# Kernel tuning notes

Measured on AMD Instinct MI355X. Metric: run time of the kernel, lower is better.

The kernel has to match this reference:

```python
import jax, jax.numpy as jnp
import numpy as np

# dims: d=1024 model width, h=16 heads, d_head=64
B, S, D, H = 4, 1024, 1024, 16
RD = float(np.sqrt(D))
VAR_W_INIT = 0.001  # var_init[0]: initial weight-variance value


def setup_inputs() -> dict:
    key = jax.random.key(0)
    ks = jax.random.split(key, 5)
    x = jax.random.normal(ks[0], (B, S, D), jnp.float32)
    # input variance must be non-negative; small positive values
    var_x = jax.random.uniform(ks[1], (B, S, D), jnp.float32) * 0.01
    scale = 1.0 / np.sqrt(D)
    Wq = jax.random.normal(ks[2], (D, D), jnp.float32) * scale
    Wk = jax.random.normal(ks[3], (D, D), jnp.float32) * scale
    Wv = jax.random.normal(ks[4], (D, D), jnp.float32) * scale
    var_Wq = jnp.full((D, D), VAR_W_INIT, jnp.float32)
    var_Wk = jnp.full((D, D), VAR_W_INIT, jnp.float32)
    var_Wv = jnp.full((D, D), VAR_W_INIT, jnp.float32)
    return dict(x=x, var_x=var_x, Wq=Wq, var_Wq=var_Wq, Wk=Wk, var_Wk=var_Wk, Wv=Wv, var_Wv=var_Wv)


def _linear_vmp(x, var_x, W, var_W):
    # mean: x W^T ; variance of product of independent Gaussians:
    # var = var_x (W^2)^T + x^2 var_W^T + var_x var_W^T
    m = x @ W.T
    v = var_x @ (W * W).T + (x * x) @ var_W.T + var_x @ var_W.T
    return m, v


def _quadratic_vmp(m1, v1, m2, v2):
    # matmul of two independent Gaussian tensors (moment propagation)
    m = m1 @ m2
    v = v1 @ v2 + v1 @ (m2 * m2) + (m1 * m1) @ v2
    return m, v


def _softmax_vmp(a, var_a):
    # delta-method through softmax: J_ij = s_i(delta_ij - s_j)
    # var_i = s_i^2 [ (1-2 s_i) var_i + sum_j s_j^2 var_j ]
    s = jax.nn.softmax(a, axis=-1)
    sv = jnp.sum(s * s * var_a, axis=-1, keepdims=True)
    var_s = s * s * ((1.0 - 2.0 * s) * var_a + sv)
    return s, var_s


def _split_heads(t):
    b, s, _ = t.shape
    return t.reshape(b, s, H, D // H).transpose(0, 2, 1, 3)  # [B,H,S,dh]


def reference(x, var_x, Wq, var_Wq, Wk, var_Wk, Wv, var_Wv):
    q, vq = _linear_vmp(x, var_x, Wq, var_Wq)
    k, vk = _linear_vmp(x, var_x, Wk, var_Wk)
    v, vv = _linear_vmp(x, var_x, Wv, var_Wv)
    q, vq, k, vk, v, vv = map(_split_heads, (q, vq, k, vk, v, vv))
    kt = k.transpose(0, 1, 3, 2)
    vkt = vk.transpose(0, 1, 3, 2)
    a, va = _quadratic_vmp(q, vq, kt, vkt)          # [B,H,S,S]
    a, va = a / RD, va / (RD * RD)
    a, va = _softmax_vmp(a, va)                      # masking=False path
    o, vo = _quadratic_vmp(a, va, v, vv)             # [B,H,S,dh]
    o = o.transpose(0, 2, 1, 3).reshape(x.shape)
    vo = vo.transpose(0, 2, 1, 3).reshape(x.shape)
    # residual_vmp, mode='identity': mean add, variances add
    return x + o, var_x + vo
```

## Files before the change

kernel.cpp:

```cpp
#include <hip/hip_runtime.h>
#include <hip/hip_bf16.h>

#define BB 4
#define SS 1024
#define DD 1024
#define HH 16
#define DH 64
#define MM (BB*SS)

typedef __attribute__((ext_vector_type(8))) short bf16x8;
typedef __attribute__((ext_vector_type(8))) unsigned short u16x8;
typedef __attribute__((ext_vector_type(4))) float f32x4;

__device__ __forceinline__ float b2f(unsigned short u) {
    union { unsigned int i; float f; } c; c.i = ((unsigned int)u) << 16; return c.f;
}
__device__ __forceinline__ unsigned short f2b(float f) {
    __hip_bfloat16 h = __float2bfloat16(f);
    return *reinterpret_cast<unsigned short*>(&h);
}
__device__ __forceinline__ unsigned int pack2(float a, float b) {
    unsigned int r;
    asm("v_cvt_pk_bf16_f32 %0, %1, %2" : "=v"(r) : "v"(a), "v"(b));
    return r;
}
__device__ __forceinline__ void gload16(const unsigned short* g, unsigned short* l) {
    __builtin_amdgcn_global_load_lds(
        (const __attribute__((address_space(1))) void*)g,
        (__attribute__((address_space(3))) void*)l,
        16, 0, 0);
}
#define MFMA16(a, b, c) __builtin_amdgcn_mfma_f32_16x16x32_bf16(a, b, c, 0, 0, 0)

__global__ __launch_bounds__(256) void prep_xw_kernel(
    const float* __restrict__ x, const float* __restrict__ vx,
    const float* __restrict__ W0, const float* __restrict__ vW0,
    const float* __restrict__ W1, const float* __restrict__ vW1,
    const float* __restrict__ W2, const float* __restrict__ vW2,
    unsigned short* __restrict__ xb, unsigned short* __restrict__ vxb,
    unsigned short* __restrict__ xsb, unsigned short* __restrict__ wp)
{
    const int gx = blockIdx.x;
    if (gx < 4096) {
        const size_t i = ((size_t)gx * 256 + threadIdx.x) * 4;
        float4 a = *(const float4*)(x + i);
        float4 b = *(const float4*)(vx + i);
        ushort4 oa = { f2b(a.x), f2b(a.y), f2b(a.z), f2b(a.w) };
        ushort4 ob = { f2b(b.x), f2b(b.y), f2b(b.z), f2b(b.w) };
        ushort4 os = { f2b(a.x*a.x), f2b(a.y*a.y), f2b(a.z*a.z), f2b(a.w*a.w) };
        *(ushort4*)(xb  + i) = oa;
        *(ushort4*)(vxb + i) = ob;
        *(ushort4*)(xsb + i) = os;
    } else {
        const int bxx = gx - 4096;
        const int z   = bxx >> 10;
        const int bx  = bxx & 1023;
        const float* W  = (z==0)? W0 : (z==1)? W1 : W2;
        const float* vW = (z==0)? vW0: (z==1)? vW1: vW2;
        const size_t NW = (size_t)DD*DD;
        unsigned short* wb = wp + (size_t)(3*z+0)*NW;
        unsigned short* wc = wp + (size_t)(3*z+1)*NW;
        unsigned short* wv = wp + (size_t)(3*z+2)*NW;
        const size_t i = ((size_t)bx * 256 + threadIdx.x) * 4;
        float4 a = *(const float4*)(W + i);
        float4 b = *(const float4*)(vW + i);
        ushort4 oa = { f2b(a.x), f2b(a.y), f2b(a.z), f2b(a.w) };
        ushort4 oc = { f2b(a.x*a.x + b.x), f2b(a.y*a.y + b.y),
                       f2b(a.z*a.z + b.z), f2b(a.w*a.w + b.w) };
        ushort4 ov = { f2b(b.x), f2b(b.y), f2b(b.z), f2b(b.w) };
        *(ushort4*)(wb + i) = oa;
        *(ushort4*)(wc + i) = oc;
        *(ushort4*)(wv + i) = ov;
    }
}

__global__ __launch_bounds__(256) void gemm_proj_kernel(
    const unsigned short* __restrict__ xb, const unsigned short* __restrict__ vxb,
    const unsigned short* __restrict__ xsb,
    const unsigned short* __restrict__ wp,
    unsigned short* __restrict__ qm, unsigned short* __restrict__ km,
    unsigned short* __restrict__ vm,
    unsigned short* __restrict__ qv, unsigned short* __restrict__ kv,
    unsigned short* __restrict__ vvv)
{
    __shared__ unsigned short sA[2][128*32];
    __shared__ unsigned short sB[2][128*32];

    const int z = blockIdx.z;
    const size_t NW = (size_t)DD*DD;
    const bool isVar = (z >= 3);
    const int p = isVar ? (z - 3) : z;
    const unsigned short* A0 = isVar ? vxb : xb;
    const unsigned short* A1 = isVar ? xsb : xb;
    const unsigned short* B0 = wp + (size_t)(3*p + (isVar ? 1 : 0)) * NW;
    const unsigned short* B1 = isVar ? (wp + (size_t)(3*p + 2) * NW) : B0;
    unsigned short* Out = (z==0)? qm : (z==1)? km : (z==2)? vm
                        : (z==3)? qv : (z==4)? kv : vvv;
    const int NT = isVar ? 64 : 32;

    const int orig = blockIdx.x + (blockIdx.y << 3);
    const int swz  = ((orig & 7) << 5) | (orig >> 3);
    const int bn = swz & 7;
    const int bm = swz >> 3;

    const int tid = threadIdx.x;
    const int w = tid >> 6;
    const int l = tid & 63;
    const int wr = w >> 1, wc = w & 1;

    const int r0 = tid >> 2;
    const int s0 = (((tid & 3) ^ ((r0 >> 1) & 3)) * 8);
    const size_t aoff0 = (size_t)(bm*128 + r0) * DD + s0;
    const size_t boff0 = (size_t)(bn*128 + r0) * DD + s0;
    const int ldsd0 = (w*64) * 8;
    const int ldsd1 = (256 + w*64) * 8;

#define STG(buf, t) do {                                                   \
        const unsigned short* As_ = ((t) < 32) ? A0 : A1;                  \
        const unsigned short* Bs_ = ((t) < 32) ? B0 : B1;                  \
        const int kc_ = ((t) & 31) * 32;                                   \
        gload16(As_ + aoff0 + kc_,                   &sA[buf][ldsd0]);     \
        gload16(As_ + aoff0 + (size_t)64*DD + kc_,   &sA[buf][ldsd1]);     \
        gload16(Bs_ + boff0 + kc_,                   &sB[buf][ldsd0]);     \
        gload16(Bs_ + boff0 + (size_t)64*DD + kc_,   &sB[buf][ldsd1]);     \
    } while (0)

    f32x4 acc[4][4];
    #pragma unroll
    for (int i = 0; i < 4; ++i)
        #pragma unroll
        for (int j = 0; j < 4; ++j)
            acc[i][j] = (f32x4){0.f,0.f,0.f,0.f};

    const int fr = l & 15;
    const int hi = l >> 4;

    STG(0, 0);
    __syncthreads();

    for (int t = 0; t < NT; ++t) {
        const int cb = t & 1;
        if (t + 1 < NT) STG(cb ^ 1, t + 1);

        bf16x8 bfr[4];
        #pragma unroll
        for (int j = 0; j < 4; ++j) {
            const int row = wc*64 + j*16 + fr;
            bfr[j] = *(const bf16x8*)&sB[cb][row*32 + ((hi ^ ((row >> 1) & 3)) * 8)];
        }
        #pragma unroll
        for (int i = 0; i < 4; ++i) {
            const int row = wr*64 + i*16 + fr;
            bf16x8 a0 = *(const bf16x8*)&sA[cb][row*32 + ((hi ^ ((row >> 1) & 3)) * 8)];
            #pragma unroll
            for (int j = 0; j < 4; ++j)
                acc[i][j] = MFMA16(a0, bfr[j], acc[i][j]);
        }
        __syncthreads();
    }
#undef STG

    const int orow = bm*128 + wr*64 + (hi << 2);
    const int ocol = bn*128 + wc*64 + fr;
    #pragma unroll
    for (int i = 0; i < 4; ++i)
        #pragma unroll
        for (int j = 0; j < 4; ++j)
            #pragma unroll
            for (int r = 0; r < 4; ++r)
                Out[(size_t)(orow + i*16 + r) * DD + ocol + j*16] = f2b(acc[i][j][r]);
}

__global__ __launch_bounds__(256) void prep_vtkk_kernel(
    const unsigned short* __restrict__ vm, const unsigned short* __restrict__ vvv,
    const unsigned short* __restrict__ kmp, const unsigned short* __restrict__ kvp,
    unsigned short* __restrict__ vt, unsigned short* __restrict__ wt,
    unsigned short* __restrict__ vvt, unsigned short* __restrict__ kkb)
{
    __shared__ unsigned short tv[64][68];
    __shared__ unsigned short tw[64][68];
    __shared__ unsigned short tvv[64][68];
    const int t = threadIdx.x;
    const int gx = blockIdx.x;

    if (gx >= 1024) {
        const size_t i = ((size_t)(gx - 1024) * 256 + t) * 8;
        u16x8 k8 = *(const u16x8*)(kmp + i);
        u16x8 v8 = *(const u16x8*)(kvp + i);
        u16x8 o8;
        #pragma unroll
        for (int e = 0; e < 8; ++e) {
            float kf = b2f(k8[e]);
            o8[e] = f2b(b2f(v8[e]) + kf*kf);
        }
        *(u16x8*)(kkb + i) = o8;
        return;
    }

    const int jt = gx & 15, h = (gx >> 4) & 15, b = gx >> 8;
    const size_t ibase = (size_t)b*SS*DD + (size_t)h*DH;
    {
        const int j = t & 63, cg = t >> 6;
        const size_t ga = ibase + (size_t)(jt*64 + j)*DD + cg*16;
        #pragma unroll
        for (int hh = 0; hh < 2; ++hh) {
            u16x8 v8  = *(const u16x8*)(vm  + ga + hh*8);
            u16x8 vv8 = *(const u16x8*)(vvv + ga + hh*8);
            u16x8 w8;
            #pragma unroll
            for (int e = 0; e < 8; ++e) {
                float vf = b2f(v8[e]);
                w8[e] = f2b(b2f(vv8[e]) + vf*vf);
            }
            *(u16x8*)&tv[j][cg*16 + hh*8]  = v8;
            *(u16x8*)&tvv[j][cg*16 + hh*8] = vv8;
            *(u16x8*)&tw[j][cg*16 + hh*8]  = w8;
        }
    }
    __syncthreads();
    {
        const int d  = t >> 2;
        const int pc = t & 3;
        const int lc = pc ^ ((d >> 1) & 3);
        #pragma unroll
        for (int st = 0; st < 2; ++st) {
            u16x8 o0, o1, o2;
            #pragma unroll
            for (int e = 0; e < 8; ++e) {
                const int jl = st*32 + (e >> 2)*16 + lc*4 + (e & 3);
                o0[e] = tv[jl][d];
                o1[e] = tw[jl][d];
                o2[e] = tvv[jl][d];
            }
            const size_t ob = (size_t)((b*HH + h)*DH + d)*SS + jt*64 + st*32 + pc*8;
            *(u16x8*)(vt  + ob) = o0;
            *(u16x8*)(wt  + ob) = o1;
            *(u16x8*)(vvt + ob) = o2;
        }
    }
}

union PW { unsigned int u[4]; bf16x8 v; };

__global__ __launch_bounds__(256, 3) void attn_mfma_kernel(
    const unsigned short* __restrict__ kmg, const unsigned short* __restrict__ kvg,
    const unsigned short* __restrict__ kkg,
    const unsigned short* __restrict__ vtg, const unsigned short* __restrict__ wtg,
    const unsigned short* __restrict__ vvtg,
    const unsigned short* __restrict__ qmg, const unsigned short* __restrict__ qvg,
    const float* __restrict__ x, const float* __restrict__ vx,
    float* __restrict__ om, float* __restrict__ ov)
{
    __shared__ unsigned short Ks[2][3][32*64];
    __shared__ unsigned short Vs[2][3][64*32];

    const int tid = threadIdx.x;
    const int w = tid >> 6, l = tid & 63;
    const int lo = l & 15, hi = l >> 4;

    const int fb = blockIdx.x;
    const int g  = ((fb >> 7) << 3) | (fb & 7);
    const int qt = (fb >> 3) & 15;
    const int h  = g & 15;
    const int b  = g >> 4;

    const size_t xbase = (size_t)b*SS*DD + (size_t)h*DH;
    const size_t vbase = (size_t)(b*HH + h)*DH*SS;

    bf16x8 qA[2], vqA[2], qsA[2];
    {
        const int qrow = qt*64 + w*16 + lo;
        #pragma unroll
        for (int ks = 0; ks < 2; ++ks) {
            const size_t ga = xbase + (size_t)qrow*DD + ks*32 + hi*8;
            qA[ks]  = *(const bf16x8*)(qmg + ga);
            vqA[ks] = *(const bf16x8*)(qvg + ga);
            #pragma unroll
            for (int e = 0; e < 8; ++e) {
                float f = b2f((unsigned short)qA[ks][e]);
                qsA[ks][e] = (short)f2b(f*f);
            }
        }
    }
    bf16x8 onesB;
    #pragma unroll
    for (int e = 0; e < 8; ++e) onesB[e] = (short)0x3F80;

    f32x4 T1[4], T2[4], T3[4], T4[4], T5[4];
    f32x4 zac = {0.f,0.f,0.f,0.f}, e2vac = {0.f,0.f,0.f,0.f};
    #pragma unroll
    for (int cb = 0; cb < 4; ++cb) {
        T1[cb] = (f32x4){0.f,0.f,0.f,0.f};
        T2[cb] = (f32x4){0.f,0.f,0.f,0.f};
        T3[cb] = (f32x4){0.f,0.f,0.f,0.f};
        T4[cb] = (f32x4){0.f,0.f,0.f,0.f};
        T5[cb] = (f32x4){0.f,0.f,0.f,0.f};
    }

    const size_t koff = (size_t)(l >> 3)*DD + (size_t)(((l & 7) ^ ((l >> 3) & 7)) * 8);
    const size_t voff = (size_t)(l >> 2)*SS + (size_t)((l & 3) * 8);

    const float KE = 0.03125f * 1.44269504f;

#define IK(bu, m, p, G) gload16(G + xbase + (j0 + (size_t)(p)*8)*DD + koff, &Ks[bu][m][(p)*512])
#define IV(bu, m, p, G) gload16(G + vbase + (size_t)((p)*16)*SS + j0 + voff, &Vs[bu][m][(p)*512])
#define STAGE(tt, bu) do {                                                     \
        const size_t j0 = (size_t)(tt) * 32;                                   \
        if (w == 0)      { IK(bu,0,0,kmg); IK(bu,0,1,kmg); IK(bu,0,2,kmg);     \
                           IK(bu,0,3,kmg); IK(bu,1,0,kvg); IK(bu,1,1,kvg); }   \
        else if (w == 1) { IK(bu,1,2,kvg); IK(bu,1,3,kvg); IK(bu,2,0,kkg);     \
                           IK(bu,2,1,kkg); IK(bu,2,2,kkg); IK(bu,2,3,kkg); }   \
        else if (w == 2) { IV(bu,0,0,vtg); IV(bu,0,1,vtg); IV(bu,0,2,vtg);     \
                           IV(bu,0,3,vtg); IV(bu,1,0,wtg); IV(bu,1,1,wtg); }   \
        else             { IV(bu,1,2,wtg); IV(bu,1,3,wtg); IV(bu,2,0,vvtg);    \
                           IV(bu,2,1,vvtg); IV(bu,2,2,vvtg); IV(bu,2,3,vvtg); }\
    } while (0)

    STAGE(0, 0);
    __syncthreads();

    int cur = 0;
    for (int t = 0; t < SS/32; ++t) {
        if (t + 1 < SS/32) STAGE(t + 1, cur ^ 1);

        PW pe, pe2, pev, pe3;
        #pragma unroll
        for (int jb = 0; jb < 2; ++jb) {
            f32x4 aa = {0.f,0.f,0.f,0.f}, vva = {0.f,0.f,0.f,0.f};
            const int jrow = jb*16 + lo;
            #pragma unroll
            for (int ks = 0; ks < 2; ++ks) {
                const int co = jrow*64 + (((ks*4 + hi) ^ (lo & 7)) * 8);
                bf16x8 kB  = *(const bf16x8*)&Ks[cur][0][co];
                bf16x8 vkB = *(const bf16x8*)&Ks[cur][1][co];
                bf16x8 kkB = *(const bf16x8*)&Ks[cur][2][co];
                aa  = MFMA16(kB,  qA[ks],  aa);
                vva = MFMA16(kkB, vqA[ks], vva);
                vva = MFMA16(vkB, qsA[ks], vva);
            }
            #pragma unroll
            for (int rp = 0; rp < 2; ++rp) {
                float e0 = exp2f(aa[rp*2]   * KE);
                float e1 = exp2f(aa[rp*2+1] * KE);
                float va0 = vva[rp*2], va1 = vva[rp*2+1];
                float s0 = e0*e0,  s1 = e1*e1;
                float v0 = s0*va0, v1 = s1*va1;
                float t0 = v0*e0,  t1 = v1*e1;
                pe.u [jb*2+rp] = pack2(e0, e1);
                pe2.u[jb*2+rp] = pack2(s0, s1);
                pev.u[jb*2+rp] = pack2(v0, v1);
                pe3.u[jb*2+rp] = pack2(t0, t1);
            }
        }

        __builtin_amdgcn_s_setprio(1);
        zac   = MFMA16(pe.v,  onesB, zac);
        e2vac = MFMA16(pev.v, onesB, e2vac);
        #pragma unroll
        for (int cb = 0; cb < 4; ++cb) {
            const int vo = (cb*16 + lo)*32 + ((hi ^ ((lo >> 1) & 3)) * 8);
            bf16x8 vB  = *(const bf16x8*)&Vs[cur][0][vo];
            bf16x8 wB  = *(const bf16x8*)&Vs[cur][1][vo];
            bf16x8 vvB = *(const bf16x8*)&Vs[cur][2][vo];
            T1[cb] = MFMA16(pe.v,  vB,  T1[cb]);
            T2[cb] = MFMA16(pev.v, wB,  T2[cb]);
            T3[cb] = MFMA16(pe3.v, wB,  T3[cb]);
            T4[cb] = MFMA16(pe2.v, wB,  T4[cb]);
            T5[cb] = MFMA16(pe2.v, vvB, T5[cb]);
        }
        __builtin_amdgcn_s_setprio(0);

        __syncthreads();
        cur ^= 1;
    }

    const float IRD2 = 0.0009765625f;
    #pragma unroll
    for (int r = 0; r < 4; ++r) {
        const float Z     = zac[r];
        const float invZ  = 1.f / Z;
        const float invZ2 = invZ * invZ;
        const float sv    = e2vac[r] * IRD2 * invZ2;
        const int row = qt*64 + w*16 + hi*4 + r;
        #pragma unroll
        for (int cb = 0; cb < 4; ++cb) {
            const size_t gi = xbase + (size_t)row*DD + cb*16 + lo;
            const float o  = T1[cb][r] * invZ;
            const float vo = (T2[cb][r]*IRD2 + sv*T4[cb][r] + T5[cb][r]) * invZ2
                           - 2.f * T3[cb][r] * IRD2 * invZ2 * invZ;
            om[gi] = x[gi] + o;
            ov[gi] = vx[gi] + vo;
        }
    }
#undef IK
#undef IV
#undef STAGE
}

extern "C" void kernel_launch(void* const* d_in, const int* in_sizes, int n_in,
                              void* d_out, int out_size, void* d_ws, size_t ws_size,
                              hipStream_t stream) {
    const float* x    = (const float*)d_in[0];
    const float* vx   = (const float*)d_in[1];
    const float* Wq   = (const float*)d_in[2];
    const float* vWq  = (const float*)d_in[3];
    const float* Wk   = (const float*)d_in[4];
    const float* vWk  = (const float*)d_in[5];
    const float* Wv   = (const float*)d_in[6];
    const float* vWv  = (const float*)d_in[7];

    const size_t NE = (size_t)MM * DD;

    unsigned short* u = (unsigned short*)d_ws;
    unsigned short* qm   = u + 0*NE;
    unsigned short* qv   = u + 1*NE;
    unsigned short* km   = u + 2*NE;
    unsigned short* kv   = u + 3*NE;
    unsigned short* vm   = u + 4*NE;
    unsigned short* vvv  = u + 5*NE;
    unsigned short* xbb  = u + 6*NE;
    unsigned short* vxbb = u + 7*NE;
    unsigned short* xsbb = u + 8*NE;
    unsigned short* wp   = u + 9*NE;

    float* om = (float*)d_out;
    float* ov = om + NE;

    prep_xw_kernel<<<7168, 256, 0, stream>>>(x, vx, Wq, vWq, Wk, vWk, Wv, vWv,
                                             xbb, vxbb, xsbb, wp);

    dim3 gg(8, 32, 6);
    gemm_proj_kernel<<<gg, 256, 0, stream>>>(xbb, vxbb, xsbb, wp,
                                             qm, km, vm, qv, kv, vvv);

    unsigned short* vt  = xbb;
    unsigned short* wt  = vxbb;
    unsigned short* vvt = xsbb;
    unsigned short* kkb = wp;
    prep_vtkk_kernel<<<3072, 256, 0, stream>>>(vm, vvv, km, kv,
                                               vt, wt, vvt, kkb);

    attn_mfma_kernel<<<1024, 256, 0, stream>>>(km, kv, kkb, vt, wt, vvt,
                                               qm, qv, x, vx, om, ov);
}
```

Measured before the change: 198.0 us.

## Triple-buffer K/V tiles with two-stage-deep async prefetch and vmcnt waits

Replaces the double-buffered K/V shared-memory pipeline with a three-buffer ring that keeps two tile loads in flight. Each step waits with an explicit vmcnt count plus a raw barrier instead of __syncthreads, so the next-next tile's loads overlap the current compute. This is meant to hide global-load latency better. The cost is a larger LDS footprint per block, which may reduce the number of resident blocks per CU.

After: 254.3 us. 1.28x slower.

```diff
diff --git a/kernel.cpp b/kernel.cpp
--- a/kernel.cpp
+++ b/kernel.cpp
@@ -251,8 +251,8 @@
     const float* __restrict__ x, const float* __restrict__ vx,
     float* __restrict__ om, float* __restrict__ ov)
 {
-    __shared__ unsigned short Ks[2][3][32*64];
-    __shared__ unsigned short Vs[2][3][64*32];
+    __shared__ unsigned short Ks[3][3][32*64];
+    __shared__ unsigned short Vs[3][3][64*32];
 
     const int tid = threadIdx.x;
     const int w = tid >> 6, l = tid & 63;
@@ -316,63 +316,70 @@
                            IV(bu,2,1,vvtg); IV(bu,2,2,vvtg); IV(bu,2,3,vvtg); }\
     } while (0)
 
+#define COMPUTE(bu) do {                                                         \
+        PW pe, pe2, pev, pe3;                                                    \
+        _Pragma("unroll")                                                        \
+        for (int jb = 0; jb < 2; ++jb) {                                         \
+            f32x4 aa = {0.f,0.f,0.f,0.f}, vva = {0.f,0.f,0.f,0.f};               \
+            const int jrow = jb*16 + lo;                                         \
+            _Pragma("unroll")                                                    \
+            for (int ks = 0; ks < 2; ++ks) {                                     \
+                const int co = jrow*64 + (((ks*4 + hi) ^ (lo & 7)) * 8);         \
+                bf16x8 kB  = *(const bf16x8*)&Ks[bu][0][co];                     \
+                bf16x8 vkB = *(const bf16x8*)&Ks[bu][1][co];                     \
+                bf16x8 kkB = *(const bf16x8*)&Ks[bu][2][co];                     \
+                aa  = MFMA16(kB,  qA[ks],  aa);                                  \
+                vva = MFMA16(kkB, vqA[ks], vva);                                 \
+                vva = MFMA16(vkB, qsA[ks], vva);                                 \
+            }                                                                    \
+            _Pragma("unroll")                                                    \
+            for (int rp = 0; rp < 2; ++rp) {                                     \
+                float e0 = exp2f(aa[rp*2]   * KE);                               \
+                float e1 = exp2f(aa[rp*2+1] * KE);                               \
+                float va0 = vva[rp*2], va1 = vva[rp*2+1];                        \
+                float s0 = e0*e0,  s1 = e1*e1;                                   \
+                float v0 = s0*va0, v1 = s1*va1;                                  \
+                float t0 = v0*e0,  t1 = v1*e1;                                   \
+                pe.u [jb*2+rp] = pack2(e0, e1);                                  \
+                pe2.u[jb*2+rp] = pack2(s0, s1);                                  \
+                pev.u[jb*2+rp] = pack2(v0, v1);                                  \
+                pe3.u[jb*2+rp] = pack2(t0, t1);                                  \
+            }                                                                    \
+        }                                                                        \
+        __builtin_amdgcn_s_setprio(1);                                           \
+        zac   = MFMA16(pe.v,  onesB, zac);                                       \
+        e2vac = MFMA16(pev.v, onesB, e2vac);                                     \
+        _Pragma("unroll")                                                        \
+        for (int cb = 0; cb < 4; ++cb) {                                         \
+            const int vo = (cb*16 + lo)*32 + ((hi ^ ((lo >> 1) & 3)) * 8);       \
+            bf16x8 vB  = *(const bf16x8*)&Vs[bu][0][vo];                         \
+            bf16x8 wB  = *(const bf16x8*)&Vs[bu][1][vo];                         \
+            bf16x8 vvB = *(const bf16x8*)&Vs[bu][2][vo];                         \
+            T1[cb] = MFMA16(pe.v,  vB,  T1[cb]);                                 \
+            T2[cb] = MFMA16(pev.v, wB,  T2[cb]);                                 \
+            T3[cb] = MFMA16(pe3.v, wB,  T3[cb]);                                 \
+            T4[cb] = MFMA16(pe2.v, wB,  T4[cb]);                                 \
+            T5[cb] = MFMA16(pe2.v, vvB, T5[cb]);                                 \
+        }                                                                        \
+        __builtin_amdgcn_s_setprio(0);                                           \
+    } while (0)
+
+#define WAITB(N) do {                                                            \
+        asm volatile("s_waitcnt vmcnt(" #N ")" ::: "memory");                    \
+        __builtin_amdgcn_s_barrier();                                            \
+        asm volatile("" ::: "memory");                                           \
+    } while (0)
+
     STAGE(0, 0);
-    __syncthreads();
-
-    int cur = 0;
-    for (int t = 0; t < SS/32; ++t) {
-        if (t + 1 < SS/32) STAGE(t + 1, cur ^ 1);
-
-        PW pe, pe2, pev, pe3;
-        #pragma unroll
-        for (int jb = 0; jb < 2; ++jb) {
-            f32x4 aa = {0.f,0.f,0.f,0.f}, vva = {0.f,0.f,0.f,0.f};
-            const int jrow = jb*16 + lo;
-            #pragma unroll
-            for (int ks = 0; ks < 2; ++ks) {
-                const int co = jrow*64 + (((ks*4 + hi) ^ (lo & 7)) * 8);
-                bf16x8 kB  = *(const bf16x8*)&Ks[cur][0][co];
-                bf16x8 vkB = *(const bf16x8*)&Ks[cur][1][co];
-                bf16x8 kkB = *(const bf16x8*)&Ks[cur][2][co];
-                aa  = MFMA16(kB,  qA[ks],  aa);
-                vva = MFMA16(kkB, vqA[ks], vva);
-                vva = MFMA16(vkB, qsA[ks], vva);
-            }
-            #pragma unroll
-            for (int rp = 0; rp < 2; ++rp) {
-                float e0 = exp2f(aa[rp*2]   * KE);
-                float e1 = exp2f(aa[rp*2+1] * KE);
-                float va0 = vva[rp*2], va1 = vva[rp*2+1];
-                float s0 = e0*e0,  s1 = e1*e1;
-                float v0 = s0*va0, v1 = s1*va1;
-                float t0 = v0*e0,  t1 = v1*e1;
-                pe.u [jb*2+rp] = pack2(e0, e1);
-                pe2.u[jb*2+rp] = pack2(s0, s1);
-                pev.u[jb*2+rp] = pack2(v0, v1);
-                pe3.u[jb*2+rp] = pack2(t0, t1);
-            }
-        }
-
-        __builtin_amdgcn_s_setprio(1);
-        zac   = MFMA16(pe.v,  onesB, zac);
-        e2vac = MFMA16(pev.v, onesB, e2vac);
-        #pragma unroll
-        for (int cb = 0; cb < 4; ++cb) {
-            const int vo = (cb*16 + lo)*32 + ((hi ^ ((lo >> 1) & 3)) * 8);
-            bf16x8 vB  = *(const bf16x8*)&Vs[cur][0][vo];
-            bf16x8 wB  = *(const bf16x8*)&Vs[cur][1][vo];
-            bf16x8 vvB = *(const bf16x8*)&Vs[cur][2][vo];
-            T1[cb] = MFMA16(pe.v,  vB,  T1[cb]);
-            T2[cb] = MFMA16(pev.v, wB,  T2[cb]);
-            T3[cb] = MFMA16(pe3.v, wB,  T3[cb]);
-            T4[cb] = MFMA16(pe2.v, wB,  T4[cb]);
-            T5[cb] = MFMA16(pe2.v, vvB, T5[cb]);
-        }
-        __builtin_amdgcn_s_setprio(0);
-
-        __syncthreads();
-        cur ^= 1;
-    }
+    STAGE(1, 1);
+
+    for (int tb = 0; tb < 30; tb += 3) {
+        WAITB(6);  STAGE(tb + 2, 2);  COMPUTE(0);
+        WAITB(6);  STAGE(tb + 3, 0);  COMPUTE(1);
+        WAITB(6);  STAGE(tb + 4, 1);  COMPUTE(2);
+    }
+    WAITB(6);  COMPUTE(0);
+    WAITB(0);  COMPUTE(1);
 
     const float IRD2 = 0.0009765625f;
     #pragma unroll
@@ -395,6 +402,8 @@
 #undef IK
 #undef IV
 #undef STAGE
+#undef COMPUTE
+#undef WAITB
 }
 
 extern "C" void kernel_launch(void* const* d_in, const int* in_sizes, int n_in,
```
